# Kernel optimization log

Measured on AMD Instinct MI355X. Metric: run time of the kernel, lower is better.

## Reference

```python
import jax, jax.numpy as jnp
import numpy as np

# Module hyperparameters (must satisfy R == T*T for the torch .view to be valid)
NUM_NODE_TYPES = 2   # T
NUM_REL_TYPES = 4    # R
NUM_BASES = 8
N_NODES = 100_000
N_EDGES = 1_600_000
IN_DIM = 64
OUT_DIM = 64
M = NUM_REL_TYPES * NUM_NODE_TYPES * NUM_NODE_TYPES  # 16 distinct relation matrices


def setup_inputs() -> dict:
    key = jax.random.key(0)
    ks = jax.random.split(key, 8)
    x = jax.random.normal(ks[0], (N_NODES, IN_DIM), dtype=jnp.float32)
    node_type = jax.random.randint(ks[1], (N_NODES,), 0, NUM_NODE_TYPES, dtype=jnp.int32)
    edge_src = jax.random.randint(ks[2], (N_EDGES,), 0, N_NODES, dtype=jnp.int32)
    edge_dst = jax.random.randint(ks[3], (N_EDGES,), 0, N_NODES, dtype=jnp.int32)
    edge_type = jax.random.randint(ks[4], (N_EDGES,), 0, NUM_REL_TYPES, dtype=jnp.int32)
    # learned params (xavier-ish scales)
    weight = jax.random.normal(ks[5], (NUM_BASES, IN_DIM, OUT_DIM), dtype=jnp.float32) * 0.05
    w_comp = jax.random.normal(ks[6], (M, NUM_BASES), dtype=jnp.float32) * 0.3
    bias = jax.random.normal(ks[7], (1, OUT_DIM), dtype=jnp.float32) * 0.1
    return {"x": x, "node_type": node_type, "edge_src": edge_src, "edge_dst": edge_dst,
            "edge_type": edge_type, "weight": weight, "w_comp": w_comp, "bias": bias}


def reference(x, node_type, edge_src, edge_dst, edge_type, weight, w_comp, bias):
    T, R = NUM_NODE_TYPES, NUM_REL_TYPES
    n_nodes = x.shape[0]
    # Faithful to torch: weight.view(out, B, in); matmul broadcasts (M,B) x (out,B,in) -> (out,M,in);
    # then .view(R*R, out, in) is a raw memory reinterpretation (valid because M == R*R).
    w_flat = weight.reshape(OUT_DIM, NUM_BASES, IN_DIM)
    comb = jnp.matmul(w_comp, w_flat)               # (out, M, in)
    W = comb.reshape(M, OUT_DIM, IN_DIM)            # (M, out, in)
    # Per-edge relation index: src_type*T*R + dst_type*R + edge_type
    rel = node_type[edge_src] * (T * R) + node_type[edge_dst] * R + edge_type  # (E,)
    # msg_e = W[rel_e] @ x[src_e]. Since there are only M=16 distinct matrices,
    # transform every node by every matrix once (N*M*out), then gather per edge;
    # same math, avoids materializing an (E,out,in) gather. Dropout is run in
    # eval mode (identity) for a deterministic reference.
    all_msgs = jnp.einsum('ni,moi->nmo', x, W)      # (N, M, out)
    msg = all_msgs[edge_src, rel]                   # (E, out)
    agg = jax.ops.segment_sum(msg, edge_dst, num_segments=n_nodes)  # (N, out)
    out = agg + bias                                # add_bias=True; activation=None
    return out
```

## Files before the change

### kernel.cpp

```cpp
#include <hip/hip_runtime.h>
#include <stdint.h>


#define TPB 256

__global__ void k_build_w(const float* __restrict__ weight,
                          const float* __restrict__ w_comp,
                          float* __restrict__ Wt, int* __restrict__ cnt) {
  const int tid = threadIdx.x;
  if (tid < 16) cnt[tid] = 0;
  for (int idx = tid; idx < 16 * 64 * 64; idx += TPB) {
    const int m = idx >> 12;
    const int i = (idx >> 6) & 63;
    const int o = idx & 63;
    const float* wc = w_comp + ((o & 15) << 3);
    const float* wf = weight + (((m << 2) + (o >> 4)) << 9) + i;
    float s = 0.f;
#pragma unroll
    for (int b = 0; b < 8; ++b) s = fmaf(wc[b], wf[b << 6], s);
    Wt[idx] = s;
  }
}

__global__ void k_hist(const int* __restrict__ nt, const int* __restrict__ esrc,
                       const int* __restrict__ edst, const int* __restrict__ etyp,
                       unsigned char* __restrict__ relRaw, int* __restrict__ cnt,
                       int E) {
  __shared__ int lc[16];
  const int tid = threadIdx.x;
  if (tid < 16) lc[tid] = 0;
  __syncthreads();
  const int e = blockIdx.x * TPB + tid;
  if (e < E) {
    const int r = nt[esrc[e]] * 8 + nt[edst[e]] * 4 + etyp[e];
    relRaw[e] = (unsigned char)r;
    atomicAdd(&lc[r], 1);
  }
  __syncthreads();
  if (tid < 16 && lc[tid]) atomicAdd(&cnt[tid], lc[tid]);
}

__global__ void k_scan(const int* __restrict__ cnt, int* __restrict__ offs,
                       int* __restrict__ cursor) {
  if (threadIdx.x == 0) {
    int run = 0;
    for (int r = 0; r < 16; ++r) { offs[r] = run; cursor[r] = run; run += cnt[r]; }
    offs[16] = run;
  }
}

__global__ void k_scatter(const int* __restrict__ esrc, const int* __restrict__ edst,
                          const unsigned char* __restrict__ relRaw,
                          int* __restrict__ cursor, int* __restrict__ srcS,
                          int* __restrict__ dstS, unsigned char* __restrict__ relS,
                          int E) {
  __shared__ int lc[16], lb[16];
  const int tid = threadIdx.x;
  if (tid < 16) lc[tid] = 0;
  __syncthreads();
  const int e = blockIdx.x * TPB + tid;
  int r = 0, lpos = 0;
  const bool ok = (e < E);
  if (ok) {
    r = relRaw[e];
    lpos = atomicAdd(&lc[r], 1);
  }
  __syncthreads();
  if (tid < 16 && lc[tid]) lb[tid] = atomicAdd(&cursor[tid], lc[tid]);
  __syncthreads();
  if (ok) {
    const int pos = lb[r] + lpos;
    srcS[pos] = esrc[e];
    dstS[pos] = edst[e];
    relS[pos] = (unsigned char)r;
  }
}

__global__ void k_init(float* __restrict__ out, const float* __restrict__ bias,
                       int total) {
  const int i = blockIdx.x * blockDim.x + threadIdx.x;
  if (i < total) out[i] = bias[i & 63];
}

__global__ __launch_bounds__(TPB) void k_gemm(
    const float* __restrict__ x, const float* __restrict__ Wt,
    const int* __restrict__ offs_g, const int* __restrict__ srcS,
    const int* __restrict__ dstS, const unsigned char* __restrict__ relS,
    float* __restrict__ out, int E) {
  __shared__ float Wl[4096];
  __shared__ float Xl[64 * 68];
  __shared__ int dstl[64];
  __shared__ int offs[17];
  const int tid = threadIdx.x;
  if (tid < 17) offs[tid] = offs_g[tid];
  __syncthreads();

  const int jb = blockIdx.x << 6;
  const int je = min(jb + 64, E);
  const int e = tid >> 2, q = tid & 3;
  const int co = tid & 15, re = tid >> 4;

  int j0 = jb;
  while (j0 < je) {
    const int r = relS[j0];
    const int j1 = min(je, offs[r + 1]);
    const int n = j1 - j0;

    {
      const float4* Wg4 = (const float4*)(Wt + (r << 12));
      float4* Wl4 = (float4*)Wl;
#pragma unroll
      for (int u = 0; u < 4; ++u) Wl4[tid + (u << 8)] = Wg4[tid + (u << 8)];
    }
    {
      float4 z = {0.f, 0.f, 0.f, 0.f};
      float4 v0 = z, v1 = z, v2 = z, v3 = z;
      if (e < n) {
        const float4* xr = (const float4*)(x + ((size_t)srcS[j0 + e] << 6)) + (q << 2);
        v0 = xr[0]; v1 = xr[1]; v2 = xr[2]; v3 = xr[3];
      }
      float* xd = &Xl[e * 68 + (q << 4)];
      *(float4*)(xd)      = v0;
      *(float4*)(xd + 4)  = v1;
      *(float4*)(xd + 8)  = v2;
      *(float4*)(xd + 12) = v3;
      if (q == 0) dstl[e] = (e < n) ? dstS[j0 + e] : -1;
    }
    __syncthreads();

    float acc[4][4] = {};
    const float* xbase = &Xl[(re << 2) * 68];
#pragma unroll 4
    for (int k4 = 0; k4 < 64; k4 += 4) {
      const float4 xv0 = *(const float4*)(xbase + k4);
      const float4 xv1 = *(const float4*)(xbase + 68 + k4);
      const float4 xv2 = *(const float4*)(xbase + 136 + k4);
      const float4 xv3 = *(const float4*)(xbase + 204 + k4);
#pragma unroll
      for (int kk = 0; kk < 4; ++kk) {
        const float4 wv = *(const float4*)&Wl[((k4 + kk) << 6) + (co << 2)];
        const float a0 = ((const float*)&xv0)[kk];
        const float a1 = ((const float*)&xv1)[kk];
        const float a2 = ((const float*)&xv2)[kk];
        const float a3 = ((const float*)&xv3)[kk];
        acc[0][0] = fmaf(a0, wv.x, acc[0][0]); acc[0][1] = fmaf(a0, wv.y, acc[0][1]);
        acc[0][2] = fmaf(a0, wv.z, acc[0][2]); acc[0][3] = fmaf(a0, wv.w, acc[0][3]);
        acc[1][0] = fmaf(a1, wv.x, acc[1][0]); acc[1][1] = fmaf(a1, wv.y, acc[1][1]);
        acc[1][2] = fmaf(a1, wv.z, acc[1][2]); acc[1][3] = fmaf(a1, wv.w, acc[1][3]);
        acc[2][0] = fmaf(a2, wv.x, acc[2][0]); acc[2][1] = fmaf(a2, wv.y, acc[2][1]);
        acc[2][2] = fmaf(a2, wv.z, acc[2][2]); acc[2][3] = fmaf(a2, wv.w, acc[2][3]);
        acc[3][0] = fmaf(a3, wv.x, acc[3][0]); acc[3][1] = fmaf(a3, wv.y, acc[3][1]);
        acc[3][2] = fmaf(a3, wv.z, acc[3][2]); acc[3][3] = fmaf(a3, wv.w, acc[3][3]);
      }
    }

#pragma unroll
    for (int j = 0; j < 4; ++j) {
      const int d = dstl[(re << 2) + j];
      if (d >= 0) {
        float* op = out + ((size_t)d << 6) + (co << 2);
        unsafeAtomicAdd(op + 0, acc[j][0]);
        unsafeAtomicAdd(op + 1, acc[j][1]);
        unsafeAtomicAdd(op + 2, acc[j][2]);
        unsafeAtomicAdd(op + 3, acc[j][3]);
      }
    }
    __syncthreads();
    j0 = j1;
  }
}

extern "C" void kernel_launch(void* const* d_in, const int* in_sizes, int n_in,
                              void* d_out, int out_size, void* d_ws, size_t ws_size,
                              hipStream_t stream) {
  const float* x      = (const float*)d_in[0];
  const int* nt       = (const int*)d_in[1];
  const int* esrc     = (const int*)d_in[2];
  const int* edst     = (const int*)d_in[3];
  const int* etyp     = (const int*)d_in[4];
  const float* weight = (const float*)d_in[5];
  const float* w_comp = (const float*)d_in[6];
  const float* bias   = (const float*)d_in[7];
  float* out = (float*)d_out;
  const int N = in_sizes[1];
  const int E = in_sizes[2];

  char* w = (char*)d_ws;
  float* Wt            = (float*)w;
  int* cnt             = (int*)(w + 262144);
  int* offs            = (int*)(w + 262144 + 256);
  int* cursor          = (int*)(w + 262144 + 512);
  int* srcS            = (int*)(w + 262912);
  int* dstS            = (int*)(w + 262912 + (size_t)E * 4);
  unsigned char* relRaw = (unsigned char*)(w + 262912 + (size_t)E * 8);
  unsigned char* relS   = relRaw + E;
  const size_t need = 262912 + (size_t)E * 10;
  if (ws_size < need) return;

  const int ebl = (E + TPB - 1) / TPB;
  const int tot = N * 64;

  hipLaunchKernelGGL(k_build_w, dim3(1), dim3(TPB), 0, stream, weight, w_comp, Wt, cnt);
  hipLaunchKernelGGL(k_hist, dim3(ebl), dim3(TPB), 0, stream, nt, esrc, edst, etyp, relRaw, cnt, E);
  hipLaunchKernelGGL(k_scan, dim3(1), dim3(64), 0, stream, cnt, offs, cursor);
  hipLaunchKernelGGL(k_scatter, dim3(ebl), dim3(TPB), 0, stream, esrc, edst, relRaw, cursor, srcS, dstS, relS, E);
  hipLaunchKernelGGL(k_init, dim3((tot + 1023) / 1024), dim3(1024), 0, stream, out, bias, tot);
  hipLaunchKernelGGL(k_gemm, dim3((E + 63) / 64), dim3(TPB), 0, stream, x, Wt, offs, srcS, dstS, relS, out, E);
}
```

Measured before the change: 1.659 ms.

## Sort edges by destination and aggregate per relation before the matmul

Replaces the relation-sorted edge GEMM that used atomic scatter with a CSR layout keyed by destination node. For each destination it sums the gathered source features into 8 per-relation buckets (src type × edge type, with dst type fixed per node), then applies the 8 relation matrices once per node and writes the output directly, adding the bias in the same pass. This removes the per-edge matmul and the float atomics on the output. In exchange it adds a node-sized histogram and a single-block scan over 100k nodes, atomic cursor scattering, and register-heavy bucketed accumulation. Reordering the summation also changes floating-point rounding.

```diff
diff --git a/kernel.cpp b/kernel.cpp
--- a/kernel.cpp
+++ b/kernel.cpp
@@ -3,170 +3,165 @@
 
 
 #define TPB 256
+#define DPB 32
+
+#define A8IDX(ld, c) (((ld) * 8 + (c)) * 76 + (((ld) & 6) << 1))
 
 __global__ void k_build_w(const float* __restrict__ weight,
                           const float* __restrict__ w_comp,
-                          float* __restrict__ Wt, int* __restrict__ cnt) {
+                          float* __restrict__ Wt) {
+  const int idx = blockIdx.x * TPB + threadIdx.x;
+  if (idx >= 16 * 64 * 64) return;
+  const int m = idx >> 12, i = (idx >> 6) & 63, o = idx & 63;
+  const float* wc = w_comp + ((o & 15) << 3);
+  const float* wf = weight + (((m << 2) + (o >> 4)) << 9) + i;
+  float s = 0.f;
+#pragma unroll
+  for (int b = 0; b < 8; ++b) s = fmaf(wc[b], wf[b << 6], s);
+  Wt[idx] = s;
+}
+
+__global__ void k_zero(int* __restrict__ p, int n) {
+  const int i = blockIdx.x * 1024 + threadIdx.x;
+  if (i < n) p[i] = 0;
+}
+
+__global__ void k_hist(const int* __restrict__ edst, int* __restrict__ cntD, int E) {
+  const int e = blockIdx.x * TPB + threadIdx.x;
+  if (e < E) atomicAdd(&cntD[edst[e]], 1);
+}
+
+#define SCAN_T 1024
+__global__ void k_scan(const int* __restrict__ cnt, int* __restrict__ offs,
+                       int* __restrict__ cursor, int N) {
+  __shared__ int ps[SCAN_T];
   const int tid = threadIdx.x;
-  if (tid < 16) cnt[tid] = 0;
-  for (int idx = tid; idx < 16 * 64 * 64; idx += TPB) {
-    const int m = idx >> 12;
-    const int i = (idx >> 6) & 63;
-    const int o = idx & 63;
-    const float* wc = w_comp + ((o & 15) << 3);
-    const float* wf = weight + (((m << 2) + (o >> 4)) << 9) + i;
-    float s = 0.f;
-#pragma unroll
-    for (int b = 0; b < 8; ++b) s = fmaf(wc[b], wf[b << 6], s);
-    Wt[idx] = s;
-  }
-}
-
-__global__ void k_hist(const int* __restrict__ nt, const int* __restrict__ esrc,
-                       const int* __restrict__ edst, const int* __restrict__ etyp,
-                       unsigned char* __restrict__ relRaw, int* __restrict__ cnt,
-                       int E) {
-  __shared__ int lc[16];
+  const int chunk = (N + SCAN_T - 1) / SCAN_T;
+  const int b = tid * chunk, e = min(b + chunk, N);
+  int s = 0;
+  for (int i = b; i < e; ++i) s += cnt[i];
+  ps[tid] = s;
+  __syncthreads();
+  for (int off = 1; off < SCAN_T; off <<= 1) {
+    int v = 0;
+    if (tid >= off) v = ps[tid - off];
+    __syncthreads();
+    ps[tid] += v;
+    __syncthreads();
+  }
+  int run = (tid > 0) ? ps[tid - 1] : 0;
+  for (int i = b; i < e; ++i) { offs[i] = run; cursor[i] = run; run += cnt[i]; }
+  if (tid == SCAN_T - 1) offs[N] = run;
+}
+
+__global__ void k_scatter(const int* __restrict__ nt, const int* __restrict__ esrc,
+                          const int* __restrict__ edst, const int* __restrict__ etyp,
+                          int* __restrict__ cursor, uint32_t* __restrict__ packS, int E) {
+  const int e = blockIdx.x * TPB + threadIdx.x;
+  if (e < E) {
+    const int s = esrc[e];
+    const uint32_t r8 = (uint32_t)(nt[s] * 4 + etyp[e]);
+    const int pos = atomicAdd(&cursor[edst[e]], 1);
+    packS[pos] = (uint32_t)s | (r8 << 24);
+  }
+}
+
+__global__ __launch_bounds__(TPB) void k_main(
+    const float* __restrict__ x, const float* __restrict__ Wt,
+    const int* __restrict__ offsD, const uint32_t* __restrict__ packS,
+    const int* __restrict__ nt, const float* __restrict__ bias,
+    float* __restrict__ out, int N) {
+  __shared__ float A8[DPB * 8 * 76 + 16];
+  __shared__ int offs[DPB + 1];
+  __shared__ int ntl[DPB];
   const int tid = threadIdx.x;
-  if (tid < 16) lc[tid] = 0;
+  const int d0 = blockIdx.x * DPB;
+  const int nd = min(DPB, N - d0);
+  if (tid <= nd) offs[tid] = offsD[d0 + tid];
+  if (tid < nd) ntl[tid] = nt[d0 + tid];
   __syncthreads();
-  const int e = blockIdx.x * TPB + tid;
-  if (e < E) {
-    const int r = nt[esrc[e]] * 8 + nt[edst[e]] * 4 + etyp[e];
-    relRaw[e] = (unsigned char)r;
-    atomicAdd(&lc[r], 1);
-  }
-  __syncthreads();
-  if (tid < 16 && lc[tid]) atomicAdd(&cnt[tid], lc[tid]);
-}
-
-__global__ void k_scan(const int* __restrict__ cnt, int* __restrict__ offs,
-                       int* __restrict__ cursor) {
-  if (threadIdx.x == 0) {
-    int run = 0;
-    for (int r = 0; r < 16; ++r) { offs[r] = run; cursor[r] = run; run += cnt[r]; }
-    offs[16] = run;
-  }
-}
-
-__global__ void k_scatter(const int* __restrict__ esrc, const int* __restrict__ edst,
-                          const unsigned char* __restrict__ relRaw,
-                          int* __restrict__ cursor, int* __restrict__ srcS,
-                          int* __restrict__ dstS, unsigned char* __restrict__ relS,
-                          int E) {
-  __shared__ int lc[16], lb[16];
-  const int tid = threadIdx.x;
-  if (tid < 16) lc[tid] = 0;
-  __syncthreads();
-  const int e = blockIdx.x * TPB + tid;
-  int r = 0, lpos = 0;
-  const bool ok = (e < E);
-  if (ok) {
-    r = relRaw[e];
-    lpos = atomicAdd(&lc[r], 1);
-  }
-  __syncthreads();
-  if (tid < 16 && lc[tid]) lb[tid] = atomicAdd(&cursor[tid], lc[tid]);
-  __syncthreads();
-  if (ok) {
-    const int pos = lb[r] + lpos;
-    srcS[pos] = esrc[e];
-    dstS[pos] = edst[e];
-    relS[pos] = (unsigned char)r;
-  }
-}
-
-__global__ void k_init(float* __restrict__ out, const float* __restrict__ bias,
-                       int total) {
-  const int i = blockIdx.x * blockDim.x + threadIdx.x;
-  if (i < total) out[i] = bias[i & 63];
-}
-
-__global__ __launch_bounds__(TPB) void k_gemm(
-    const float* __restrict__ x, const float* __restrict__ Wt,
-    const int* __restrict__ offs_g, const int* __restrict__ srcS,
-    const int* __restrict__ dstS, const unsigned char* __restrict__ relS,
-    float* __restrict__ out, int E) {
-  __shared__ float Wl[4096];
-  __shared__ float Xl[64 * 68];
-  __shared__ int dstl[64];
-  __shared__ int offs[17];
-  const int tid = threadIdx.x;
-  if (tid < 17) offs[tid] = offs_g[tid];
-  __syncthreads();
-
-  const int jb = blockIdx.x << 6;
-  const int je = min(jb + 64, E);
-  const int e = tid >> 2, q = tid & 3;
-  const int co = tid & 15, re = tid >> 4;
-
-  int j0 = jb;
-  while (j0 < je) {
-    const int r = relS[j0];
-    const int j1 = min(je, offs[r + 1]);
-    const int n = j1 - j0;
-
-    {
-      const float4* Wg4 = (const float4*)(Wt + (r << 12));
-      float4* Wl4 = (float4*)Wl;
-#pragma unroll
-      for (int u = 0; u < 4; ++u) Wl4[tid + (u << 8)] = Wg4[tid + (u << 8)];
-    }
-    {
-      float4 z = {0.f, 0.f, 0.f, 0.f};
-      float4 v0 = z, v1 = z, v2 = z, v3 = z;
-      if (e < n) {
-        const float4* xr = (const float4*)(x + ((size_t)srcS[j0 + e] << 6)) + (q << 2);
-        v0 = xr[0]; v1 = xr[1]; v2 = xr[2]; v3 = xr[3];
-      }
-      float* xd = &Xl[e * 68 + (q << 4)];
-      *(float4*)(xd)      = v0;
-      *(float4*)(xd + 4)  = v1;
-      *(float4*)(xd + 8)  = v2;
-      *(float4*)(xd + 12) = v3;
-      if (q == 0) dstl[e] = (e < n) ? dstS[j0 + e] : -1;
-    }
-    __syncthreads();
-
-    float acc[4][4] = {};
-    const float* xbase = &Xl[(re << 2) * 68];
-#pragma unroll 4
-    for (int k4 = 0; k4 < 64; k4 += 4) {
-      const float4 xv0 = *(const float4*)(xbase + k4);
-      const float4 xv1 = *(const float4*)(xbase + 68 + k4);
-      const float4 xv2 = *(const float4*)(xbase + 136 + k4);
-      const float4 xv3 = *(const float4*)(xbase + 204 + k4);
-#pragma unroll
-      for (int kk = 0; kk < 4; ++kk) {
-        const float4 wv = *(const float4*)&Wl[((k4 + kk) << 6) + (co << 2)];
-        const float a0 = ((const float*)&xv0)[kk];
-        const float a1 = ((const float*)&xv1)[kk];
-        const float a2 = ((const float*)&xv2)[kk];
-        const float a3 = ((const float*)&xv3)[kk];
-        acc[0][0] = fmaf(a0, wv.x, acc[0][0]); acc[0][1] = fmaf(a0, wv.y, acc[0][1]);
-        acc[0][2] = fmaf(a0, wv.z, acc[0][2]); acc[0][3] = fmaf(a0, wv.w, acc[0][3]);
-        acc[1][0] = fmaf(a1, wv.x, acc[1][0]); acc[1][1] = fmaf(a1, wv.y, acc[1][1]);
-        acc[1][2] = fmaf(a1, wv.z, acc[1][2]); acc[1][3] = fmaf(a1, wv.w, acc[1][3]);
-        acc[2][0] = fmaf(a2, wv.x, acc[2][0]); acc[2][1] = fmaf(a2, wv.y, acc[2][1]);
-        acc[2][2] = fmaf(a2, wv.z, acc[2][2]); acc[2][3] = fmaf(a2, wv.w, acc[2][3]);
-        acc[3][0] = fmaf(a3, wv.x, acc[3][0]); acc[3][1] = fmaf(a3, wv.y, acc[3][1]);
-        acc[3][2] = fmaf(a3, wv.z, acc[3][2]); acc[3][3] = fmaf(a3, wv.w, acc[3][3]);
+
+  const int w = tid >> 6, lane = tid & 63;
+  for (int ld = w; ld < DPB; ld += 4) {
+    float racc[8] = {0.f, 0.f, 0.f, 0.f, 0.f, 0.f, 0.f, 0.f};
+    if (ld < nd) {
+      const int j0 = offs[ld], j1 = offs[ld + 1];
+      for (int j = j0; j < j1; j += 8) {
+        uint32_t pk[8];
+        float xv[8];
+#pragma unroll
+        for (int u = 0; u < 8; ++u) {
+          const int jj = min(j + u, j1 - 1);
+          pk[u] = packS[jj];
+        }
+#pragma unroll
+        for (int u = 0; u < 8; ++u)
+          xv[u] = x[((size_t)(pk[u] & 0x00FFFFFFu) << 6) + lane];
+#pragma unroll
+        for (int u = 0; u < 8; ++u) {
+          const float v = (j + u < j1) ? xv[u] : 0.f;
+          switch (pk[u] >> 24) {
+            case 0: racc[0] += v; break;
+            case 1: racc[1] += v; break;
+            case 2: racc[2] += v; break;
+            case 3: racc[3] += v; break;
+            case 4: racc[4] += v; break;
+            case 5: racc[5] += v; break;
+            case 6: racc[6] += v; break;
+            default: racc[7] += v; break;
+          }
+        }
       }
     }
-
-#pragma unroll
-    for (int j = 0; j < 4; ++j) {
-      const int d = dstl[(re << 2) + j];
-      if (d >= 0) {
-        float* op = out + ((size_t)d << 6) + (co << 2);
-        unsafeAtomicAdd(op + 0, acc[j][0]);
-        unsafeAtomicAdd(op + 1, acc[j][1]);
-        unsafeAtomicAdd(op + 2, acc[j][2]);
-        unsafeAtomicAdd(op + 3, acc[j][3]);
+#pragma unroll
+    for (int c = 0; c < 8; ++c) A8[A8IDX(ld, c) + lane] = racc[c];
+  }
+  __syncthreads();
+
+  const int co = tid & 15, re = tid >> 4;
+  const int ld0 = re * 2, ld1 = re * 2 + 1;
+  float acc[2][4];
+#pragma unroll
+  for (int j = 0; j < 4; ++j) {
+    const float bv = bias[(co << 2) + j];
+    acc[0][j] = bv;
+    acc[1][j] = bv;
+  }
+  const int t0 = (ld0 < nd) ? ntl[ld0] : 0;
+  const int t1 = (ld1 < nd) ? ntl[ld1] : 0;
+  const float4* Wt4 = (const float4*)Wt;
+#pragma unroll 2
+  for (int r8 = 0; r8 < 8; ++r8) {
+    const int rel0 = ((r8 >> 2) << 3) + (t0 << 2) + (r8 & 3);
+    const int rel1 = ((r8 >> 2) << 3) + (t1 << 2) + (r8 & 3);
+    const float4* wp0 = Wt4 + (rel0 << 10) + co;
+    const float4* wp1 = Wt4 + (rel1 << 10) + co;
+    const float* a0 = &A8[A8IDX(ld0, r8)];
+    const float* a1 = &A8[A8IDX(ld1, r8)];
+    for (int k4 = 0; k4 < 64; k4 += 4) {
+      const float4 av0 = *(const float4*)(a0 + k4);
+      const float4 av1 = *(const float4*)(a1 + k4);
+#pragma unroll
+      for (int kk = 0; kk < 4; ++kk) {
+        const float4 w0 = wp0[(k4 + kk) << 4];
+        const float4 w1 = wp1[(k4 + kk) << 4];
+        const float f0 = ((const float*)&av0)[kk];
+        const float f1 = ((const float*)&av1)[kk];
+        acc[0][0] = fmaf(f0, w0.x, acc[0][0]); acc[0][1] = fmaf(f0, w0.y, acc[0][1]);
+        acc[0][2] = fmaf(f0, w0.z, acc[0][2]); acc[0][3] = fmaf(f0, w0.w, acc[0][3]);
+        acc[1][0] = fmaf(f1, w1.x, acc[1][0]); acc[1][1] = fmaf(f1, w1.y, acc[1][1]);
+        acc[1][2] = fmaf(f1, w1.z, acc[1][2]); acc[1][3] = fmaf(f1, w1.w, acc[1][3]);
       }
     }
-    __syncthreads();
-    j0 = j1;
+  }
+
+  if (ld0 < nd) {
+    float4 v = {acc[0][0], acc[0][1], acc[0][2], acc[0][3]};
+    *(float4*)(out + ((size_t)(d0 + ld0) << 6) + (co << 2)) = v;
+  }
+  if (ld1 < nd) {
+    float4 v = {acc[1][0], acc[1][1], acc[1][2], acc[1][3]};
+    *(float4*)(out + ((size_t)(d0 + ld1) << 6) + (co << 2)) = v;
   }
 }
 
@@ -185,25 +180,23 @@
   const int N = in_sizes[1];
   const int E = in_sizes[2];
 
-  char* w = (char*)d_ws;
-  float* Wt            = (float*)w;
-  int* cnt             = (int*)(w + 262144);
-  int* offs            = (int*)(w + 262144 + 256);
-  int* cursor          = (int*)(w + 262144 + 512);
-  int* srcS            = (int*)(w + 262912);
-  int* dstS            = (int*)(w + 262912 + (size_t)E * 4);
-  unsigned char* relRaw = (unsigned char*)(w + 262912 + (size_t)E * 8);
-  unsigned char* relS   = relRaw + E;
-  const size_t need = 262912 + (size_t)E * 10;
-  if (ws_size < need) return;
+  char* wsp = (char*)d_ws;
+  size_t off = 0;
+  float* Wt = (float*)(wsp + off); off += 262144;
+  int* cntD = (int*)(wsp + off); off += (size_t)N * 4;
+  int* offsD = (int*)(wsp + off); off += (size_t)(N + 1) * 4 + 12;
+  int* cursor = (int*)(wsp + off); off += (size_t)N * 4;
+  uint32_t* packS = (uint32_t*)(wsp + off); off += (size_t)E * 4;
+  if (ws_size < off) return;
 
   const int ebl = (E + TPB - 1) / TPB;
-  const int tot = N * 64;
-
-  hipLaunchKernelGGL(k_build_w, dim3(1), dim3(TPB), 0, stream, weight, w_comp, Wt, cnt);
-  hipLaunchKernelGGL(k_hist, dim3(ebl), dim3(TPB), 0, stream, nt, esrc, edst, etyp, relRaw, cnt, E);
-  hipLaunchKernelGGL(k_scan, dim3(1), dim3(64), 0, stream, cnt, offs, cursor);
-  hipLaunchKernelGGL(k_scatter, dim3(ebl), dim3(TPB), 0, stream, esrc, edst, relRaw, cursor, srcS, dstS, relS, E);
-  hipLaunchKernelGGL(k_init, dim3((tot + 1023) / 1024), dim3(1024), 0, stream, out, bias, tot);
-  hipLaunchKernelGGL(k_gemm, dim3((E + 63) / 64), dim3(TPB), 0, stream, x, Wt, offs, srcS, dstS, relS, out, E);
-}
+
+  hipLaunchKernelGGL(k_zero, dim3((N + 1023) / 1024), dim3(1024), 0, stream, cntD, N);
+  hipLaunchKernelGGL(k_build_w, dim3(256), dim3(TPB), 0, stream, weight, w_comp, Wt);
+  hipLaunchKernelGGL(k_hist, dim3(ebl), dim3(TPB), 0, stream, edst, cntD, E);
+  hipLaunchKernelGGL(k_scan, dim3(1), dim3(SCAN_T), 0, stream, cntD, offsD, cursor, N);
+  hipLaunchKernelGGL(k_scatter, dim3(ebl), dim3(TPB), 0, stream, nt, esrc, edst, etyp,
+                     cursor, packS, E);
+  hipLaunchKernelGGL(k_main, dim3((N + DPB - 1) / DPB), dim3(TPB), 0, stream,
+                     x, Wt, offsD, packS, nt, bias, out, N);
+}
```

Result: slower. 1.758 ms (+6.0%).
